# Optimization experiments

Hardware: AMD Instinct MI355X
Metric: run time of the kernel (lower is better)

## Reference

```python
import jax, jax.numpy as jnp
import numpy as np

KSIZE = 11
SIGMA = 1.5
PAD = KSIZE // 2
C1 = 0.01 ** 2
C2 = 0.03 ** 2


def gaussian_kernel(ksize, sigma):
    ax = np.arange(ksize, dtype=np.float32) - (ksize - 1) / 2.0
    g = np.exp(-(ax ** 2) / (2.0 * sigma ** 2))
    k2d = np.outer(g, g)
    k2d = k2d / k2d.sum()
    # depthwise kernel for 3 channels: [out=3, in/groups=1, kh, kw]
    return jnp.asarray(np.broadcast_to(k2d, (3, 1, ksize, ksize)).copy())


def dwconv(x, kernel):
    # x: [B,3,H,W], kernel: [3,1,k,k], 'same' padding, groups=3
    return jax.lax.conv_general_dilated(
        x, kernel,
        window_strides=(1, 1),
        padding=[(PAD, PAD), (PAD, PAD)],
        dimension_numbers=('NCHW', 'OIHW', 'NCHW'),
        feature_group_count=3)


def setup_inputs() -> dict:
    key = jax.random.key(0)
    k1, k2 = jax.random.split(key)
    shape = (16, 3, 512, 512)
    img_output = jax.random.uniform(k1, shape, dtype=jnp.float32)
    img_target = jax.random.uniform(k2, shape, dtype=jnp.float32)
    kernel = gaussian_kernel(KSIZE, SIGMA)
    return {"img_output": img_output, "img_target": img_target, "kernel": kernel}


def reference(img_output, img_target, kernel):
    s, t = img_output, img_target
    ux = dwconv(s, kernel)
    uy = dwconv(t, kernel)
    uxx = dwconv(s * s, kernel)
    uyy = dwconv(t * t, kernel)
    uxy = dwconv(s * t, kernel)
    ssim = ((2 * ux * uy + C1) * (2 * (uxy - ux * uy) + C2)
            / (ux ** 2 + uy ** 2 + C1)
            / (uxx - ux * ux + (uyy - uy * uy) + C2))
    return 1.0 - ssim.mean()
```

## Files before the change

kernel.cpp:

```cpp
#include <hip/hip_runtime.h>

typedef _Float16 f16;
typedef f16  f16x8 __attribute__((ext_vector_type(8)));
typedef f16  f16x2 __attribute__((ext_vector_type(2)));
typedef float f32x4 __attribute__((ext_vector_type(4)));

#define W 512
#define H 512
#define KS 11
#define ROWS 48
#define PITCH 18
#define NW 4
#define NBLK 6144
#define NLINES 256
#define C1_SSIM 0.0001f
#define C2_SSIM 0.0009f
#define NTOTAL 12582912.0f

__device__ __constant__ const float GW[KS] = {
    1.02838e-3f, 7.59876e-3f, 3.600076e-2f, 1.0936069e-1f, 2.1300554e-1f,
    2.6601172e-1f,
    2.1300554e-1f, 1.0936069e-1f, 3.600076e-2f, 7.59876e-3f, 1.02838e-3f
};

__device__ inline float ssim_px(float ux, float uy, float uxx, float uyy, float uxy) {
    const float uxuy = ux * uy;
    const float a = 2.f * uxuy + C1_SSIM;
    const float b = 2.f * (uxy - uxuy) + C2_SSIM;
    const float c = ux * ux + uy * uy + C1_SSIM;
    const float d = (uxx - ux * ux) + (uyy - uy * uy) + C2_SSIM;
    return (a * b) * __builtin_amdgcn_rcpf(c * d);
}

struct __attribute__((aligned(4))) F4 { float x, y, z, w; };

__device__ __forceinline__ void load8f(const float* __restrict__ base, int ry,
                                       int xs, float v[8]) {
    if ((unsigned)ry < (unsigned)H) {
        const float* r = base + ((size_t)ry << 9);
        if ((unsigned)xs <= (unsigned)(W - 8)) {
            const F4 a = *(const F4*)(r + xs);
            const F4 b = *(const F4*)(r + xs + 4);
            v[0] = a.x; v[1] = a.y; v[2] = a.z; v[3] = a.w;
            v[4] = b.x; v[5] = b.y; v[6] = b.z; v[7] = b.w;
        } else {
            #pragma unroll
            for (int j = 0; j < 8; ++j) {
                const int x = xs + j;
                v[j] = ((unsigned)x < (unsigned)W) ? r[x] : 0.f;
            }
        }
    } else {
        #pragma unroll
        for (int j = 0; j < 8; ++j) v[j] = 0.f;
    }
}

__global__ __launch_bounds__(256)
void ssim_main(const float* __restrict__ simg, const float* __restrict__ timg,
               float* __restrict__ accum) {
    __shared__ f16 hsh[NW][5][ROWS][PITCH];
    __shared__ float red[NW];

    const int tid  = threadIdx.x;
    const int w    = tid >> 6;
    const int lane = tid & 63;
    const int n    = lane & 15;
    const int q    = lane >> 4;

    const int L  = blockIdx.x * NW + w;
    const int z  = L >> 9;
    const int r  = L & 511;
    const int ty = r >> 5;
    const int tx = r & 31;

    const float* sp = simg + ((size_t)z << 18);
    const float* tp = timg + ((size_t)z << 18);
    const int x0 = tx << 4;
    const int y0 = (ty << 5) - 5;
    const int xs = x0 - 5 + (q << 3);

    f16x8 af;
    #pragma unroll
    for (int j = 0; j < 8; ++j) {
        const int k = (q << 3) + j;
        const int d = k - n;
        af[j] = (d >= 0 && d < KS) ? (f16)GW[d] : (f16)0.f;
    }

    f16x8 sf[3], tf[3];
    #pragma unroll
    for (int g = 0; g < 3; ++g) {
        float v[8];
        load8f(sp, y0 + (g << 4) + n, xs, v);
        #pragma unroll
        for (int j = 0; j < 8; ++j) sf[g][j] = (f16)v[j];
        load8f(tp, y0 + (g << 4) + n, xs, v);
        #pragma unroll
        for (int j = 0; j < 8; ++j) tf[g][j] = (f16)v[j];
    }

    #pragma unroll
    for (int g = 0; g < 3; ++g) {
        f16x8 bb[5];
        bb[0] = sf[g];
        bb[1] = tf[g];
        bb[2] = sf[g] * sf[g];
        bb[3] = tf[g] * tf[g];
        bb[4] = sf[g] * tf[g];
        #pragma unroll
        for (int c = 0; c < 5; ++c) {
            const f32x4 zero = {0.f, 0.f, 0.f, 0.f};
            const f32x4 d = __builtin_amdgcn_mfma_f32_16x16x32_f16(af, bb[c], zero, 0, 0, 0);
            f16x2 p;
            p[0] = (f16)d[0]; p[1] = (f16)d[1];
            *(f16x2*)&hsh[w][c][(g << 4) + n][(q << 2)]     = p;
            p[0] = (f16)d[2]; p[1] = (f16)d[3];
            *(f16x2*)&hsh[w][c][(g << 4) + n][(q << 2) + 2] = p;
        }
    }

    f32x4 acc[2][5];
    #pragma unroll
    for (int t = 0; t < 2; ++t) {
        #pragma unroll
        for (int c = 0; c < 5; ++c) {
            f16x8 bf;
            #pragma unroll
            for (int j = 0; j < 8; ++j)
                bf[j] = hsh[w][c][(t << 4) + (q << 3) + j][n];
            const f32x4 zero = {0.f, 0.f, 0.f, 0.f};
            acc[t][c] = __builtin_amdgcn_mfma_f32_16x16x32_f16(af, bf, zero, 0, 0, 0);
        }
    }

    float sum = 0.f;
    #pragma unroll
    for (int t = 0; t < 2; ++t)
        #pragma unroll
        for (int rg = 0; rg < 4; ++rg)
            sum += ssim_px(acc[t][0][rg], acc[t][1][rg], acc[t][2][rg],
                           acc[t][3][rg], acc[t][4][rg]);
    #pragma unroll
    for (int off = 32; off > 0; off >>= 1)
        sum += __shfl_down(sum, off, 64);
    if (lane == 0) red[w] = sum;
    __syncthreads();
    if (tid == 0) {
        atomicAdd(&accum[(blockIdx.x & (NLINES - 1)) << 4],
                  red[0] + red[1] + red[2] + red[3]);
    }
}

__global__ void ssim_final(const float* __restrict__ accum, float* __restrict__ out) {
    const int lane = threadIdx.x;
    float s = 0.f;
    #pragma unroll
    for (int i = 0; i < NLINES / 64; ++i)
        s += accum[((i << 6) + lane) << 4];
    #pragma unroll
    for (int off = 32; off > 0; off >>= 1)
        s += __shfl_down(s, off, 64);
    if (lane == 0) out[0] = 1.f - s * (1.f / NTOTAL);
}

extern "C" void kernel_launch(void* const* d_in, const int* in_sizes, int n_in,
                              void* d_out, int out_size, void* d_ws, size_t ws_size,
                              hipStream_t stream) {
    const float* s = (const float*)d_in[0];
    const float* t = (const float*)d_in[1];
    float* out   = (float*)d_out;
    float* accum = (float*)d_ws;

    hipMemsetAsync(accum, 0, NLINES * 16 * sizeof(float), stream);
    ssim_main<<<dim3(NBLK), 256, 0, stream>>>(s, t, accum);
    ssim_final<<<1, 64, 0, stream>>>(accum, out);
}
```

Baseline: 155.2 us.

## Replace LDS transpose between separable MFMA passes with register shuffles

The horizontal pass now computes the MFMA with swapped operands, so each lane holds outputs in the row layout the vertical pass needs. The intermediate is then redistributed with cross-lane shuffles instead of a round trip through shared memory. This drops the LDS staging array and its 2-byte strided reads. It also switches the f16 conversions to packed cvt_pkrtz and sets launch bounds to target 5 blocks per SIMD. In exchange it issues many ds_bpermute shuffles and uses more registers.

```diff
diff --git a/kernel.cpp b/kernel.cpp
--- a/kernel.cpp
+++ b/kernel.cpp
@@ -8,8 +8,6 @@
 #define W 512
 #define H 512
 #define KS 11
-#define ROWS 48
-#define PITCH 18
 #define NW 4
 #define NBLK 6144
 #define NLINES 256
@@ -22,6 +20,8 @@
     2.6601172e-1f,
     2.1300554e-1f, 1.0936069e-1f, 3.600076e-2f, 7.59876e-3f, 1.02838e-3f
 };
+
+union B32 { f16x2 h; int i; };
 
 __device__ inline float ssim_px(float ux, float uy, float uxx, float uyy, float uxy) {
     const float uxuy = ux * uy;
@@ -56,10 +56,21 @@
     }
 }
 
-__global__ __launch_bounds__(256)
+__device__ __forceinline__ f16x8 pack8(const float v[8]) {
+    f16x8 r;
+    #pragma unroll
+    for (int p = 0; p < 4; ++p) {
+        const f16x2 h = __builtin_bit_cast(
+            f16x2, __builtin_amdgcn_cvt_pkrtz(v[2 * p], v[2 * p + 1]));
+        r[2 * p]     = h[0];
+        r[2 * p + 1] = h[1];
+    }
+    return r;
+}
+
+__global__ __launch_bounds__(256, 5)
 void ssim_main(const float* __restrict__ simg, const float* __restrict__ timg,
                float* __restrict__ accum) {
-    __shared__ f16 hsh[NW][5][ROWS][PITCH];
     __shared__ float red[NW];
 
     const int tid  = threadIdx.x;
@@ -88,59 +99,65 @@
         af[j] = (d >= 0 && d < KS) ? (f16)GW[d] : (f16)0.f;
     }
 
-    f16x8 sf[3], tf[3];
+    const int LA = n | ((q & 1) << 5);
+    const int LB = LA | 16;
+
+    B32 ph[3][5][2];
     #pragma unroll
     for (int g = 0; g < 3; ++g) {
         float v[8];
         load8f(sp, y0 + (g << 4) + n, xs, v);
-        #pragma unroll
-        for (int j = 0; j < 8; ++j) sf[g][j] = (f16)v[j];
+        const f16x8 sf = pack8(v);
         load8f(tp, y0 + (g << 4) + n, xs, v);
-        #pragma unroll
-        for (int j = 0; j < 8; ++j) tf[g][j] = (f16)v[j];
-    }
-
-    #pragma unroll
-    for (int g = 0; g < 3; ++g) {
-        f16x8 bb[5];
-        bb[0] = sf[g];
-        bb[1] = tf[g];
-        bb[2] = sf[g] * sf[g];
-        bb[3] = tf[g] * tf[g];
-        bb[4] = sf[g] * tf[g];
+        const f16x8 tf = pack8(v);
         #pragma unroll
         for (int c = 0; c < 5; ++c) {
+            f16x8 ch;
+            if      (c == 0) ch = sf;
+            else if (c == 1) ch = tf;
+            else if (c == 2) ch = sf * sf;
+            else if (c == 3) ch = tf * tf;
+            else             ch = sf * tf;
             const f32x4 zero = {0.f, 0.f, 0.f, 0.f};
-            const f32x4 d = __builtin_amdgcn_mfma_f32_16x16x32_f16(af, bb[c], zero, 0, 0, 0);
-            f16x2 p;
-            p[0] = (f16)d[0]; p[1] = (f16)d[1];
-            *(f16x2*)&hsh[w][c][(g << 4) + n][(q << 2)]     = p;
-            p[0] = (f16)d[2]; p[1] = (f16)d[3];
-            *(f16x2*)&hsh[w][c][(g << 4) + n][(q << 2) + 2] = p;
-        }
-    }
-
-    f32x4 acc[2][5];
-    #pragma unroll
-    for (int t = 0; t < 2; ++t) {
-        #pragma unroll
-        for (int c = 0; c < 5; ++c) {
-            f16x8 bf;
-            #pragma unroll
-            for (int j = 0; j < 8; ++j)
-                bf[j] = hsh[w][c][(t << 4) + (q << 3) + j][n];
-            const f32x4 zero = {0.f, 0.f, 0.f, 0.f};
-            acc[t][c] = __builtin_amdgcn_mfma_f32_16x16x32_f16(af, bf, zero, 0, 0, 0);
+            const f32x4 d = __builtin_amdgcn_mfma_f32_16x16x32_f16(ch, af, zero, 0, 0, 0);
+            ph[g][c][0].h = __builtin_bit_cast(f16x2, __builtin_amdgcn_cvt_pkrtz(d[0], d[1]));
+            ph[g][c][1].h = __builtin_bit_cast(f16x2, __builtin_amdgcn_cvt_pkrtz(d[2], d[3]));
         }
     }
 
     float sum = 0.f;
     #pragma unroll
-    for (int t = 0; t < 2; ++t)
+    for (int t = 0; t < 2; ++t) {
+        f32x4 acc[5];
+        #pragma unroll
+        for (int c = 0; c < 5; ++c) {
+            B32 a0, a1, a2, a3, b0, b1, b2, b3, r0, r1, r2, r3;
+            a0.i = __shfl(ph[t][c][0].i,     LA, 64);
+            a1.i = __shfl(ph[t][c][1].i,     LA, 64);
+            a2.i = __shfl(ph[t][c][0].i,     LB, 64);
+            a3.i = __shfl(ph[t][c][1].i,     LB, 64);
+            b0.i = __shfl(ph[t + 1][c][0].i, LA, 64);
+            b1.i = __shfl(ph[t + 1][c][1].i, LA, 64);
+            b2.i = __shfl(ph[t + 1][c][0].i, LB, 64);
+            b3.i = __shfl(ph[t + 1][c][1].i, LB, 64);
+            const bool lo = (q < 2);
+            r0.i = lo ? a0.i : b0.i;
+            r1.i = lo ? a1.i : b1.i;
+            r2.i = lo ? a2.i : b2.i;
+            r3.i = lo ? a3.i : b3.i;
+            f16x8 bf;
+            bf[0] = r0.h[0]; bf[1] = r0.h[1];
+            bf[2] = r1.h[0]; bf[3] = r1.h[1];
+            bf[4] = r2.h[0]; bf[5] = r2.h[1];
+            bf[6] = r3.h[0]; bf[7] = r3.h[1];
+            const f32x4 zero = {0.f, 0.f, 0.f, 0.f};
+            acc[c] = __builtin_amdgcn_mfma_f32_16x16x32_f16(af, bf, zero, 0, 0, 0);
+        }
         #pragma unroll
         for (int rg = 0; rg < 4; ++rg)
-            sum += ssim_px(acc[t][0][rg], acc[t][1][rg], acc[t][2][rg],
-                           acc[t][3][rg], acc[t][4][rg]);
+            sum += ssim_px(acc[0][rg], acc[1][rg], acc[2][rg], acc[3][rg], acc[4][rg]);
+    }
+
     #pragma unroll
     for (int off = 32; off > 0; off >>= 1)
         sum += __shfl_down(sum, off, 64);
```

New measurement: 151.7 us. -2.3%, faster.
